# Kernel optimization log

Hardware: AMD Instinct MI355X
Metric: run time of the kernel (lower is better)

## Reference

```python
import jax, jax.numpy as jnp
import numpy as np

N_SAMPLES = 8_000_000
NB_CLASSES = 5


def setup_inputs() -> dict:
    key = jax.random.key(0)
    k1, k2 = jax.random.split(key)
    preds = jax.random.normal(k1, (N_SAMPLES, NB_CLASSES), dtype=jnp.float32)
    true = jax.random.randint(k2, (N_SAMPLES,), 0, NB_CLASSES, dtype=jnp.int32)
    return {"preds": preds, "true": true}


def reference(preds, true):
    N, C = preds.shape
    dt = preds.dtype
    cls = jnp.arange(C, dtype=dt)

    # SoftArgmax1D per row (base_index=0, step_size=1), then round -> hard class
    soft_arg = jax.nn.softmax(preds, axis=1) @ cls            # [N]
    pred_idx = jnp.clip(jnp.round(soft_arg).astype(jnp.int32), 0, C - 1)

    # confusion_matrix[true, pred] += 1 via fused scatter-add on flat index
    flat = true * C + pred_idx                                 # [N]
    conf = jnp.zeros((C * C,), dtype=dt).at[flat].add(1.0).reshape(C, C)

    # quadratic kappa weights: (i-j)^2 / (C-1)^2
    weights = (cls[:, None] - cls[None, :]) ** 2 / ((C - 1) ** 2)

    # class histograms (scatter-add)
    true_hist = jnp.zeros((C,), dtype=dt).at[true].add(1.0)
    pred_hist = jnp.zeros((C,), dtype=dt).at[pred_idx].add(1.0)

    # expected matrix E = outer(true_hist, pred_hist), both normalized
    E = jnp.outer(true_hist, pred_hist)
    E = E / E.sum()
    conf = conf / conf.sum()

    num = (conf * weights).sum()
    den = (E * weights).sum()
    return num / den
```

## Files before the change

kernel.cpp:

```cpp
#include <hip/hip_runtime.h>
#include <math.h>

#define NCLS 5
#define NBINS 25
#define NBLOCKS 512
#define NTHREADS 256

__global__ void __launch_bounds__(NTHREADS)
kappa_count(const float* __restrict__ preds,
            const int* __restrict__ truev,
            int N,
            unsigned int* __restrict__ partials) {
    __shared__ unsigned int s_conf[NBINS];
    const int tid = threadIdx.x;
    if (tid < NBINS) s_conf[tid] = 0u;
    __syncthreads();

    const int nquad = N >> 2;
    const int gstride = gridDim.x * blockDim.x;
    for (int q = blockIdx.x * blockDim.x + tid; q < nquad; q += gstride) {
        const float4* p4 = (const float4*)(preds + (size_t)q * 20u);
        float4 a = p4[0];
        float4 b = p4[1];
        float4 c = p4[2];
        float4 d = p4[3];
        float4 e = p4[4];
        int4 t4 = *(const int4*)(truev + (size_t)q * 4u);

        float rows[4][NCLS] = {
            {a.x, a.y, a.z, a.w, b.x},
            {b.y, b.z, b.w, c.x, c.y},
            {c.z, c.w, d.x, d.y, d.z},
            {d.w, e.x, e.y, e.z, e.w}
        };
        int ts[4] = {t4.x, t4.y, t4.z, t4.w};

        #pragma unroll
        for (int r = 0; r < 4; r++) {
            float m = rows[r][0];
            #pragma unroll
            for (int j = 1; j < NCLS; j++) m = fmaxf(m, rows[r][j]);
            float s = 0.f, dot = 0.f;
            #pragma unroll
            for (int j = 0; j < NCLS; j++) {
                float ex = __expf(rows[r][j] - m);
                s += ex;
                dot += ex * (float)j;
            }
            int pi = (int)rintf(dot / s);
            pi = min(max(pi, 0), NCLS - 1);
            atomicAdd(&s_conf[ts[r] * NCLS + pi], 1u);
        }
    }

    if (blockIdx.x == 0 && tid < (N & 3)) {
        int i = (N & ~3) + tid;
        float v[NCLS];
        #pragma unroll
        for (int j = 0; j < NCLS; j++) v[j] = preds[(size_t)i * NCLS + j];
        float m = v[0];
        #pragma unroll
        for (int j = 1; j < NCLS; j++) m = fmaxf(m, v[j]);
        float s = 0.f, dot = 0.f;
        #pragma unroll
        for (int j = 0; j < NCLS; j++) {
            float ex = __expf(v[j] - m);
            s += ex;
            dot += ex * (float)j;
        }
        int pi = (int)rintf(dot / s);
        pi = min(max(pi, 0), NCLS - 1);
        atomicAdd(&s_conf[truev[i] * NCLS + pi], 1u);
    }

    __syncthreads();
    if (tid < NBINS) partials[blockIdx.x * NBINS + tid] = s_conf[tid];
}

__global__ void kappa_final(const unsigned int* __restrict__ partials,
                            int nblocks,
                            float* __restrict__ out) {
    __shared__ unsigned int s_conf[NBINS];
    const int tid = threadIdx.x;
    if (tid < NBINS) s_conf[tid] = 0u;
    __syncthreads();

    const int total = nblocks * NBINS;
    for (int i = tid; i < total; i += blockDim.x) {
        unsigned int v = partials[i];
        if (v) atomicAdd(&s_conf[i % NBINS], v);
    }
    __syncthreads();

    if (tid == 0) {
        double conf[NBINS];
        double tot = 0.0;
        for (int i = 0; i < NBINS; i++) { conf[i] = (double)s_conf[i]; tot += conf[i]; }
        double th[NCLS] = {0, 0, 0, 0, 0};
        double ph[NCLS] = {0, 0, 0, 0, 0};
        for (int i = 0; i < NCLS; i++)
            for (int j = 0; j < NCLS; j++) {
                th[i] += conf[i * NCLS + j];
                ph[j] += conf[i * NCLS + j];
            }
        double num = 0.0, den = 0.0;
        for (int i = 0; i < NCLS; i++)
            for (int j = 0; j < NCLS; j++) {
                double w = (double)((i - j) * (i - j)) / 16.0;
                num += w * conf[i * NCLS + j];
                den += w * th[i] * ph[j];
            }
        out[0] = (float)(num * tot / den);
    }
}

extern "C" void kernel_launch(void* const* d_in, const int* in_sizes, int n_in,
                              void* d_out, int out_size, void* d_ws, size_t ws_size,
                              hipStream_t stream) {
    const float* preds = (const float*)d_in[0];
    const int* truev = (const int*)d_in[1];
    const int N = in_sizes[1];

    int nblocks = NBLOCKS;
    size_t need = (size_t)nblocks * NBINS * sizeof(unsigned int);
    if (need > ws_size) nblocks = (int)(ws_size / (NBINS * sizeof(unsigned int)));
    unsigned int* partials = (unsigned int*)d_ws;

    kappa_count<<<nblocks, NTHREADS, 0, stream>>>(preds, truev, N, partials);
    kappa_final<<<1, 256, 0, stream>>>(partials, nblocks, (float*)d_out);
}
```

Before: 257.2 us.

## Prefetch next quad, per-wave LDS histograms, more blocks, transposed partials reduction

The main loop now loads the next iteration's 20 floats and 4 labels before working on the current ones, so memory latency can overlap with the softmax arithmetic. Each wave gets its own shared-memory histogram to reduce atomic contention. The grid grows to 4096 blocks with a launch-bounds occupancy hint. Partials are stored bin-major so the final kernel can sum each bin with one 32-lane shuffle reduction instead of shared atomics. The risks are higher register pressure from the prefetch and a larger partials buffer to reduce.

```diff
diff --git a/kernel.cpp b/kernel.cpp
--- a/kernel.cpp
+++ b/kernel.cpp
@@ -3,111 +3,110 @@
 
 #define NCLS 5
 #define NBINS 25
-#define NBLOCKS 512
 #define NTHREADS 256
+#define NBLOCKS 4096
 
-__global__ void __launch_bounds__(NTHREADS)
+__global__ void __launch_bounds__(NTHREADS, 4)
 kappa_count(const float* __restrict__ preds,
             const int* __restrict__ truev,
             int N,
             unsigned int* __restrict__ partials) {
-    __shared__ unsigned int s_conf[NBINS];
+    __shared__ unsigned int s_conf[4 * 32];
     const int tid = threadIdx.x;
-    if (tid < NBINS) s_conf[tid] = 0u;
+    const int wv = tid >> 6;
+    if (tid < 128) s_conf[tid] = 0u;
     __syncthreads();
+    unsigned int* hist = &s_conf[wv << 5];
+
+    auto dorow = [&](float r0, float r1, float r2, float r3, float r4, int t) {
+        float m = fmaxf(fmaxf(fmaxf(fmaxf(r0, r1), r2), r3), r4);
+        float e0 = __expf(r0 - m), e1 = __expf(r1 - m), e2 = __expf(r2 - m),
+              e3 = __expf(r3 - m), e4 = __expf(r4 - m);
+        float s = e0 + e1 + e2 + e3 + e4;
+        float dot = e1 + e2 * 2.f + e3 * 3.f + e4 * 4.f;
+        int pi = (int)rintf(dot / s);
+        pi = min(max(pi, 0), NCLS - 1);
+        atomicAdd(&hist[t * NCLS + pi], 1u);
+    };
 
     const int nquad = N >> 2;
-    const int gstride = gridDim.x * blockDim.x;
-    for (int q = blockIdx.x * blockDim.x + tid; q < nquad; q += gstride) {
-        const float4* p4 = (const float4*)(preds + (size_t)q * 20u);
-        float4 a = p4[0];
-        float4 b = p4[1];
-        float4 c = p4[2];
-        float4 d = p4[3];
-        float4 e = p4[4];
+    const int gs = gridDim.x * blockDim.x;
+
+    int q = blockIdx.x * blockDim.x + tid;
+    if (q < nquad) {
+        const float4* p4 = (const float4*)preds + (size_t)q * 5u;
+        float4 a = p4[0], b = p4[1], c = p4[2], d = p4[3], e = p4[4];
         int4 t4 = *(const int4*)(truev + (size_t)q * 4u);
-
-        float rows[4][NCLS] = {
-            {a.x, a.y, a.z, a.w, b.x},
-            {b.y, b.z, b.w, c.x, c.y},
-            {c.z, c.w, d.x, d.y, d.z},
-            {d.w, e.x, e.y, e.z, e.w}
-        };
-        int ts[4] = {t4.x, t4.y, t4.z, t4.w};
-
-        #pragma unroll
-        for (int r = 0; r < 4; r++) {
-            float m = rows[r][0];
-            #pragma unroll
-            for (int j = 1; j < NCLS; j++) m = fmaxf(m, rows[r][j]);
-            float s = 0.f, dot = 0.f;
-            #pragma unroll
-            for (int j = 0; j < NCLS; j++) {
-                float ex = __expf(rows[r][j] - m);
-                s += ex;
-                dot += ex * (float)j;
+        for (;;) {
+            const int qn = q + gs;
+            const bool more = qn < nquad;
+            float4 an, bn, cn, dn, en;
+            int4 tn;
+            if (more) {
+                const float4* pn = (const float4*)preds + (size_t)qn * 5u;
+                an = pn[0]; bn = pn[1]; cn = pn[2]; dn = pn[3]; en = pn[4];
+                tn = *(const int4*)(truev + (size_t)qn * 4u);
             }
-            int pi = (int)rintf(dot / s);
-            pi = min(max(pi, 0), NCLS - 1);
-            atomicAdd(&s_conf[ts[r] * NCLS + pi], 1u);
+            dorow(a.x, a.y, a.z, a.w, b.x, t4.x);
+            dorow(b.y, b.z, b.w, c.x, c.y, t4.y);
+            dorow(c.z, c.w, d.x, d.y, d.z, t4.z);
+            dorow(d.w, e.x, e.y, e.z, e.w, t4.w);
+            if (!more) break;
+            a = an; b = bn; c = cn; d = dn; e = en; t4 = tn;
+            q = qn;
         }
     }
 
     if (blockIdx.x == 0 && tid < (N & 3)) {
-        int i = (N & ~3) + tid;
+        const int i = (N & ~3) + tid;
         float v[NCLS];
         #pragma unroll
         for (int j = 0; j < NCLS; j++) v[j] = preds[(size_t)i * NCLS + j];
-        float m = v[0];
-        #pragma unroll
-        for (int j = 1; j < NCLS; j++) m = fmaxf(m, v[j]);
-        float s = 0.f, dot = 0.f;
-        #pragma unroll
-        for (int j = 0; j < NCLS; j++) {
-            float ex = __expf(v[j] - m);
-            s += ex;
-            dot += ex * (float)j;
-        }
-        int pi = (int)rintf(dot / s);
-        pi = min(max(pi, 0), NCLS - 1);
-        atomicAdd(&s_conf[truev[i] * NCLS + pi], 1u);
+        dorow(v[0], v[1], v[2], v[3], v[4], truev[i]);
     }
 
     __syncthreads();
-    if (tid < NBINS) partials[blockIdx.x * NBINS + tid] = s_conf[tid];
+    if (tid < NBINS) {
+        unsigned int v = s_conf[tid] + s_conf[32 + tid] +
+                         s_conf[64 + tid] + s_conf[96 + tid];
+        partials[(size_t)tid * gridDim.x + blockIdx.x] = v;
+    }
 }
 
 __global__ void kappa_final(const unsigned int* __restrict__ partials,
-                            int nblocks,
+                            int nb,
                             float* __restrict__ out) {
-    __shared__ unsigned int s_conf[NBINS];
+    __shared__ double s_bin[NBINS];
     const int tid = threadIdx.x;
-    if (tid < NBINS) s_conf[tid] = 0u;
-    __syncthreads();
+    const int bin = tid >> 5;
+    const int l = tid & 31;
 
-    const int total = nblocks * NBINS;
-    for (int i = tid; i < total; i += blockDim.x) {
-        unsigned int v = partials[i];
-        if (v) atomicAdd(&s_conf[i % NBINS], v);
+    if (bin < NBINS) {
+        unsigned int acc = 0u;
+        const unsigned int* p = partials + (size_t)bin * nb;
+        for (int j = l; j < nb; j += 32) acc += p[j];
+        #pragma unroll
+        for (int off = 16; off > 0; off >>= 1)
+            acc += __shfl_down(acc, off, 32);
+        if (l == 0) s_bin[bin] = (double)acc;
     }
     __syncthreads();
 
     if (tid == 0) {
-        double conf[NBINS];
         double tot = 0.0;
-        for (int i = 0; i < NBINS; i++) { conf[i] = (double)s_conf[i]; tot += conf[i]; }
+        for (int i = 0; i < NBINS; i++) tot += s_bin[i];
         double th[NCLS] = {0, 0, 0, 0, 0};
         double ph[NCLS] = {0, 0, 0, 0, 0};
         for (int i = 0; i < NCLS; i++)
             for (int j = 0; j < NCLS; j++) {
-                th[i] += conf[i * NCLS + j];
-                ph[j] += conf[i * NCLS + j];
+                th[i] += s_bin[i * NCLS + j];
+                ph[j] += s_bin[i * NCLS + j];
             }
         double num = 0.0, den = 0.0;
         for (int i = 0; i < NCLS; i++)
             for (int j = 0; j < NCLS; j++) {
                 double w = (double)((i - j) * (i - j)) / 16.0;
-                num += w * conf[i * NCLS + j];
+                num += w * s_bin[i * NCLS + j];
                 den += w * th[i] * ph[j];
             }
         out[0] = (float)(num * tot / den);
@@ -127,5 +126,5 @@
     unsigned int* partials = (unsigned int*)d_ws;
 
     kappa_count<<<nblocks, NTHREADS, 0, stream>>>(preds, truev, N, partials);
-    kappa_final<<<1, 256, 0, stream>>>(partials, nblocks, (float*)d_out);
+    kappa_final<<<1, 1024, 0, stream>>>(partials, nblocks, (float*)d_out);
 }
```

Measured after the change: 259.5 us. No clear change (+0.9%).
